# Performance work log

Measured on AMD Instinct MI355X. Metric: run time of the kernel, lower is better.

Reference implementation:

```python
import jax, jax.numpy as jnp
import numpy as np

N_ATOMS = 200000
N_BONDS = 300000
E = 600000
D = 128
H = 128
EPS = 1e-5  # BatchNorm1d default eps


def setup_inputs() -> dict:
    key = jax.random.key(0)
    ks = jax.random.split(key, 8)
    x_atoms = jax.random.normal(ks[0], (N_ATOMS, D), jnp.float32)
    x_bonds = jax.random.normal(ks[1], (N_BONDS, D), jnp.float32)
    # atoms -> bonds edges: row0 src atom idx, row1 dst bond idx
    ei_ab = jnp.stack([
        jax.random.randint(ks[2], (E,), 0, N_ATOMS),
        jax.random.randint(ks[3], (E,), 0, N_BONDS),
    ]).astype(jnp.int64)
    # bonds -> atoms edges
    ei_ba = jnp.stack([
        jax.random.randint(ks[4], (E,), 0, N_BONDS),
        jax.random.randint(ks[5], (E,), 0, N_ATOMS),
    ]).astype(jnp.int64)
    xav = float(np.sqrt(6.0 / (D + H)))
    W = jax.random.uniform(ks[6], (H, D), jnp.float32, -xav, xav)   # shared lin_rel
    b = jnp.zeros((H,), jnp.float32)
    Wr = jax.random.uniform(ks[7], (H, D), jnp.float32, -xav, xav)  # res_connection
    br = jnp.zeros((H,), jnp.float32)
    return {
        "x_atoms": x_atoms, "x_bonds": x_bonds,
        "ei_ab": ei_ab, "ei_ba": ei_ba,
        "W": W, "b": b, "Wr": Wr, "br": br,
        "gamma_atoms": jnp.ones((H,), jnp.float32),
        "beta_atoms": jnp.zeros((H,), jnp.float32),
        "gamma_bonds": jnp.ones((H,), jnp.float32),
        "beta_bonds": jnp.zeros((H,), jnp.float32),
    }


def _bn(v, g, bt):
    # BatchNorm1d training-mode math: batch mean, biased variance
    m = v.mean(axis=0)
    var = v.var(axis=0)
    return (v - m) * jax.lax.rsqrt(var + EPS) * g + bt


def reference(x_atoms, x_bonds, ei_ab, ei_ba, W, b, Wr, br,
              gamma_atoms, beta_atoms, gamma_bonds, beta_bonds):
    # shared lin_rel applied to both node types
    h_atoms = x_atoms @ W.T + b   # [N_ATOMS, H]
    h_bonds = x_bonds @ W.T + b   # [N_BONDS, H]

    # message = lin(x_src)[src], aggregate = scatter-add at dst (source_to_target)
    agg_bonds = jax.ops.segment_sum(h_atoms[ei_ab[0]], ei_ab[1], num_segments=N_BONDS)
    agg_atoms = jax.ops.segment_sum(h_bonds[ei_ba[0]], ei_ba[1], num_segments=N_ATOMS)

    # residual: activation(res_connection(x))
    out_atoms = agg_atoms + jax.nn.relu(x_atoms @ Wr.T + br)
    out_bonds = agg_bonds + jax.nn.relu(x_bonds @ Wr.T + br)

    # dropout is identity in eval/deterministic reference
    out_atoms = _bn(out_atoms, gamma_atoms, beta_atoms)
    out_bonds = _bn(out_bonds, gamma_bonds, beta_bonds)
    return out_atoms, out_bonds
```

## Files before the change

### kernel.cpp

```cpp
#include <hip/hip_runtime.h>
#include <stdint.h>

#define NATOMS 200000
#define NBONDS 300000
#define NEDGE  600000
#define NSEG   (NATOMS + NBONDS)
#define DF     128
#define EPS    1e-5f
#define SCHUNK 2048
#define NSBLK  ((NSEG + SCHUNK - 1) / SCHUNK)
#define NBUCK  32
#define NCHA   (NATOMS / 64)
#define NCHB   ((NBONDS + 63) / 64)
#define NCH    (NCHA + NCHB)

typedef __attribute__((ext_vector_type(8))) short bf16x8;
typedef __attribute__((ext_vector_type(4))) float f32x4;
typedef unsigned short u16;

__device__ __forceinline__ short f2b(float f) {
  union { float f; uint32_t u; } v; v.f = f;
  uint32_t r = v.u + 0x7fffu + ((v.u >> 16) & 1u);
  return (short)(r >> 16);
}
__device__ __forceinline__ float bf2f(u16 h) {
  union { uint32_t u; float f; } v; v.u = ((uint32_t)h) << 16; return v.f;
}
__device__ __forceinline__ bf16x8 pack8(float4 u, float4 v) {
  bf16x8 t;
  t[0] = f2b(u.x); t[1] = f2b(u.y); t[2] = f2b(u.z); t[3] = f2b(u.w);
  t[4] = f2b(v.x); t[5] = f2b(v.y); t[6] = f2b(v.z); t[7] = f2b(v.w);
  return t;
}

__global__ void k_prep(const float* __restrict__ W, const float* __restrict__ Wr,
                       u16* __restrict__ Wb, u16* __restrict__ Wrb) {
  int i = blockIdx.x * blockDim.x + threadIdx.x;
  if (i < DF * DF) {
    Wb[i]  = (u16)f2b(W[i]);
    Wrb[i] = (u16)f2b(Wr[i]);
  }
}

__global__ void k_setup(const float* __restrict__ xa, const float* __restrict__ xb,
                        u16* __restrict__ xaT, u16* __restrict__ xbT,
                        const int* __restrict__ ab, const int* __restrict__ ba,
                        int* __restrict__ cnt,
                        const float* __restrict__ W, const float* __restrict__ Wr,
                        u16* __restrict__ Wb, u16* __restrict__ Wrb) {
  const int NA8 = NATOMS * DF / 8;
  const int NT8 = NSEG * DF / 8;
  int bid = blockIdx.x;
  if (bid < 4096) {
    int stride = 4096 * 256;
    for (int i = bid * 256 + threadIdx.x; i < NT8; i += stride) {
      const float* src; u16* dst; int j;
      if (i < NA8) { src = xa; dst = xaT; j = i; }
      else { src = xb; dst = xbT; j = i - NA8; }
      const float4 a = *(const float4*)(src + (size_t)j * 8);
      const float4 b = *(const float4*)(src + (size_t)j * 8 + 4);
      *(bf16x8*)(dst + (size_t)j * 8) = pack8(a, b);
    }
  } else if (bid < 4608) {
    int stride = 512 * 256;
    for (int e = (bid - 4096) * 256 + threadIdx.x; e < 2 * NEDGE; e += stride) {
      int g;
      if (e < NEDGE) g = NATOMS + ab[NEDGE + e];
      else           g = ba[NEDGE + (e - NEDGE)];
      atomicAdd(cnt + g, 1);
    }
  } else {
    int i = (bid - 4608) * 256 + threadIdx.x;
    if (i < DF * DF) {
      Wb[i]  = (u16)f2b(W[i]);
      Wrb[i] = (u16)f2b(Wr[i]);
    }
  }
}

__global__ void k_hist(const int* __restrict__ ab, const int* __restrict__ ba,
                       int* __restrict__ cnt) {
  int stride = gridDim.x * blockDim.x;
  for (int e = blockIdx.x * blockDim.x + threadIdx.x; e < 2 * NEDGE; e += stride) {
    int g;
    if (e < NEDGE) g = NATOMS + ab[NEDGE + e];
    else           g = ba[NEDGE + (e - NEDGE)];
    atomicAdd(cnt + g, 1);
  }
}

__global__ void k_scanA(const int* __restrict__ cnt, int* __restrict__ bsum) {
  __shared__ int wsm[4];
  int t = threadIdx.x;
  int base = blockIdx.x * SCHUNK + t * 8;
  int s = 0;
#pragma unroll
  for (int j = 0; j < 8; ++j) { int i = base + j; if (i < NSEG) s += cnt[i]; }
  for (int d = 1; d < 64; d <<= 1) s += __shfl_xor(s, d);
  if ((t & 63) == 0) wsm[t >> 6] = s;
  __syncthreads();
  if (t == 0) bsum[blockIdx.x] = wsm[0] + wsm[1] + wsm[2] + wsm[3];
}

__global__ void k_scanB(const int* __restrict__ bsum, int* __restrict__ bbase) {
  __shared__ int wsm[4];
  int t = threadIdx.x;
  int lane = t & 63;
  int v = (t < NSBLK) ? bsum[t] : 0;
  int s = v;
  for (int d = 1; d < 64; d <<= 1) { int n = __shfl_up(s, d); if (lane >= d) s += n; }
  if (lane == 63) wsm[t >> 6] = s;
  __syncthreads();
  int wbase = 0;
  for (int w = 0; w < (t >> 6); ++w) wbase += wsm[w];
  if (t < NSBLK) bbase[t] = wbase + s - v;
}

__global__ void k_scanC(const int* __restrict__ cnt, const int* __restrict__ bbase,
                        int* __restrict__ off, int* __restrict__ cursor) {
  __shared__ int wsm[4];
  int t = threadIdx.x;
  int lane = t & 63, wv = t >> 6;
  int base = blockIdx.x * SCHUNK + t * 8;
  int v[8]; int ts = 0;
#pragma unroll
  for (int j = 0; j < 8; ++j) { int i = base + j; v[j] = (i < NSEG) ? cnt[i] : 0; ts += v[j]; }
  int s = ts;
  for (int d = 1; d < 64; d <<= 1) { int n = __shfl_up(s, d); if (lane >= d) s += n; }
  if (lane == 63) wsm[wv] = s;
  __syncthreads();
  int wbase = bbase[blockIdx.x];
  for (int w = 0; w < wv; ++w) wbase += wsm[w];
  int run = wbase + s - ts;
#pragma unroll
  for (int j = 0; j < 8; ++j) {
    int i = base + j;
    if (i < NSEG) { off[i] = run; cursor[i] = run; }
    run += v[j];
  }
}

__global__ void k_fill(const int* __restrict__ ab, const int* __restrict__ ba,
                       int* __restrict__ cursor, int* __restrict__ sorted) {
  int stride = gridDim.x * blockDim.x;
  for (int e = blockIdx.x * blockDim.x + threadIdx.x; e < 2 * NEDGE; e += stride) {
    int g, src;
    if (e < NEDGE) { g = NATOMS + ab[NEDGE + e]; src = ab[e]; }
    else { int e2 = e - NEDGE; g = ba[NEDGE + e2]; src = ba[e2]; }
    int pos = atomicAdd(cursor + g, 1);
    sorted[pos] = src;
  }
}

__global__ __launch_bounds__(256, 2) void k_fuse(
    const u16* __restrict__ xaT, const u16* __restrict__ xbT,
    const int* __restrict__ sorted, const int* __restrict__ off,
    const int* __restrict__ cnt, u16* __restrict__ gT,
    const u16* __restrict__ Wb, const u16* __restrict__ Wrb,
    const float* __restrict__ bb, const float* __restrict__ brb,
    float* __restrict__ stats) {
  __shared__ u16 aggL[64 * DF];

  int tid = threadIdx.x;
  int lane = tid & 63;
  int wv = tid >> 6;
  int r16 = lane & 15, kq = lane >> 4;
  int t016 = wv * 32;
  int qw = tid >> 4;
  int l16 = tid & 15;

  bf16x8 wf[2][4], wrf[2][4];
#pragma unroll
  for (int ti = 0; ti < 2; ++ti) {
#pragma unroll
    for (int kk = 0; kk < 4; ++kk) {
      size_t o = (size_t)(t016 + ti * 16 + r16) * DF + kk * 32 + kq * 8;
      wf[ti][kk]  = *(const bf16x8*)(Wb + o);
      wrf[ti][kk] = *(const bf16x8*)(Wrb + o);
    }
  }
  float bvv0 = bb[t016 + r16],      brr0 = brb[t016 + r16];
  float bvv1 = bb[t016 + 16 + r16], brr1 = brb[t016 + 16 + r16];

  float sA0 = 0.f, sA1 = 0.f, qA0 = 0.f, qA1 = 0.f;
  float sB0 = 0.f, sB1 = 0.f, qB0 = 0.f, qB1 = 0.f;

  for (int c = blockIdx.x; c < NCH; c += gridDim.x) {
    int typ, nrows, goff, base;
    if (c < NCHA) { typ = 0; nrows = NATOMS; goff = 0; base = c * 64; }
    else { typ = 1; nrows = NBONDS; goff = NATOMS; base = (c - NCHA) * 64; }
    const u16* gsrc = typ ? xaT : xbT;
    const u16* xsrc = typ ? xbT : xaT;

    __syncthreads();

#pragma unroll
    for (int i = 0; i < 4; ++i) {
      int r = qw + i * 16;
      int row = base + r;
      if (row < nrows) {
        int gidx = goff + row;
        int start = off[gidx], deg = cnt[gidx];
        float a0 = 0.f, a1 = 0.f, a2 = 0.f, a3 = 0.f;
        float a4 = 0.f, a5 = 0.f, a6 = 0.f, a7 = 0.f;
        int k = 0;
        for (; k + 1 < deg; k += 2) {
          int s0 = sorted[start + k], s1 = sorted[start + k + 1];
          bf16x8 v0 = *(const bf16x8*)(gsrc + (size_t)s0 * DF + l16 * 8);
          bf16x8 v1 = *(const bf16x8*)(gsrc + (size_t)s1 * DF + l16 * 8);
          a0 += bf2f((u16)v0[0]) + bf2f((u16)v1[0]);
          a1 += bf2f((u16)v0[1]) + bf2f((u16)v1[1]);
          a2 += bf2f((u16)v0[2]) + bf2f((u16)v1[2]);
          a3 += bf2f((u16)v0[3]) + bf2f((u16)v1[3]);
          a4 += bf2f((u16)v0[4]) + bf2f((u16)v1[4]);
          a5 += bf2f((u16)v0[5]) + bf2f((u16)v1[5]);
          a6 += bf2f((u16)v0[6]) + bf2f((u16)v1[6]);
          a7 += bf2f((u16)v0[7]) + bf2f((u16)v1[7]);
        }
        if (k < deg) {
          int s0 = sorted[start + k];
          bf16x8 v0 = *(const bf16x8*)(gsrc + (size_t)s0 * DF + l16 * 8);
          a0 += bf2f((u16)v0[0]); a1 += bf2f((u16)v0[1]);
          a2 += bf2f((u16)v0[2]); a3 += bf2f((u16)v0[3]);
          a4 += bf2f((u16)v0[4]); a5 += bf2f((u16)v0[5]);
          a6 += bf2f((u16)v0[6]); a7 += bf2f((u16)v0[7]);
        }
        bf16x8 rr;
        rr[0] = f2b(a0); rr[1] = f2b(a1); rr[2] = f2b(a2); rr[3] = f2b(a3);
        rr[4] = f2b(a4); rr[5] = f2b(a5); rr[6] = f2b(a6); rr[7] = f2b(a7);
        *(bf16x8*)(aggL + r * DF + ((l16 ^ (r & 7)) * 8)) = rr;
      }
    }
    __syncthreads();

#pragma unroll
    for (int rg = 0; rg < 4; ++rg) {
      int rowbase = base + rg * 16;
      if (rowbase < nrows) {
        int lrow = rg * 16 + r16;
        bf16x8 fA[4], fX[4];
#pragma unroll
        for (int kk = 0; kk < 4; ++kk) {
          int c8 = (4 * kk + kq) ^ (r16 & 7);
          fA[kk] = *(const bf16x8*)(aggL + lrow * DF + c8 * 8);
        }
        const u16* xp = xsrc + (size_t)(rowbase + r16) * DF + kq * 8;
#pragma unroll
        for (int kk = 0; kk < 4; ++kk) fX[kk] = *(const bf16x8*)(xp + kk * 32);

        f32x4 w0 = {0.f,0.f,0.f,0.f}, w1 = {0.f,0.f,0.f,0.f};
        f32x4 r0 = {0.f,0.f,0.f,0.f}, r1 = {0.f,0.f,0.f,0.f};
#pragma unroll
        for (int kk = 0; kk < 4; ++kk) {
          w0 = __builtin_amdgcn_mfma_f32_16x16x32_bf16(fA[kk], wf[0][kk], w0, 0, 0, 0);
          w1 = __builtin_amdgcn_mfma_f32_16x16x32_bf16(fA[kk], wf[1][kk], w1, 0, 0, 0);
          r0 = __builtin_amdgcn_mfma_f32_16x16x32_bf16(fX[kk], wrf[0][kk], r0, 0, 0, 0);
          r1 = __builtin_amdgcn_mfma_f32_16x16x32_bf16(fX[kk], wrf[1][kk], r1, 0, 0, 0);
        }

        float cf0 = (float)cnt[goff + rowbase + kq * 4 + 0];
        float cf1 = (float)cnt[goff + rowbase + kq * 4 + 1];
        float cf2 = (float)cnt[goff + rowbase + kq * 4 + 2];
        float cf3 = (float)cnt[goff + rowbase + kq * 4 + 3];

        u16* gp = gT + ((size_t)(goff + rowbase + kq * 4) << 7) + t016 + r16;
        float g0, g1, g2, g3, ss, qq;
        g0 = w0[0] + cf0 * bvv0 + fmaxf(r0[0] + brr0, 0.f);
        g1 = w0[1] + cf1 * bvv0 + fmaxf(r0[1] + brr0, 0.f);
        g2 = w0[2] + cf2 * bvv0 + fmaxf(r0[2] + brr0, 0.f);
        g3 = w0[3] + cf3 * bvv0 + fmaxf(r0[3] + brr0, 0.f);
        gp[0]   = (u16)f2b(g0); gp[128] = (u16)f2b(g1);
        gp[256] = (u16)f2b(g2); gp[384] = (u16)f2b(g3);
        ss = g0 + g1 + g2 + g3;
        qq = g0*g0 + g1*g1 + g2*g2 + g3*g3;
        if (typ) { sB0 += ss; qB0 += qq; } else { sA0 += ss; qA0 += qq; }
        g0 = w1[0] + cf0 * bvv1 + fmaxf(r1[0] + brr1, 0.f);
        g1 = w1[1] + cf1 * bvv1 + fmaxf(r1[1] + brr1, 0.f);
        g2 = w1[2] + cf2 * bvv1 + fmaxf(r1[2] + brr1, 0.f);
        g3 = w1[3] + cf3 * bvv1 + fmaxf(r1[3] + brr1, 0.f);
        gp[16]  = (u16)f2b(g0); gp[144] = (u16)f2b(g1);
        gp[272] = (u16)f2b(g2); gp[400] = (u16)f2b(g3);
        ss = g0 + g1 + g2 + g3;
        qq = g0*g0 + g1*g1 + g2*g2 + g3*g3;
        if (typ) { sB1 += ss; qB1 += qq; } else { sA1 += ss; qA1 += qq; }
      }
    }
  }

  int bkt = blockIdx.x & (NBUCK - 1);
  float* p = stats + (size_t)bkt * 4 * DF;
  {
    float s0 = sA0, q0 = qA0, s1 = sB0, q1 = qB0;
    s0 += __shfl_xor(s0, 16); q0 += __shfl_xor(q0, 16);
    s1 += __shfl_xor(s1, 16); q1 += __shfl_xor(q1, 16);
    s0 += __shfl_xor(s0, 32); q0 += __shfl_xor(q0, 32);
    s1 += __shfl_xor(s1, 32); q1 += __shfl_xor(q1, 32);
    if (kq == 0) {
      int feat = t016 + r16;
      atomicAdd(p + 0 * DF + feat, s0);
      atomicAdd(p + 1 * DF + feat, q0);
      atomicAdd(p + 2 * DF + feat, s1);
      atomicAdd(p + 3 * DF + feat, q1);
    }
  }
  {
    float s0 = sA1, q0 = qA1, s1 = sB1, q1 = qB1;
    s0 += __shfl_xor(s0, 16); q0 += __shfl_xor(q0, 16);
    s1 += __shfl_xor(s1, 16); q1 += __shfl_xor(q1, 16);
    s0 += __shfl_xor(s0, 32); q0 += __shfl_xor(q0, 32);
    s1 += __shfl_xor(s1, 32); q1 += __shfl_xor(q1, 32);
    if (kq == 0) {
      int feat = t016 + 16 + r16;
      atomicAdd(p + 0 * DF + feat, s0);
      atomicAdd(p + 1 * DF + feat, q0);
      atomicAdd(p + 2 * DF + feat, s1);
      atomicAdd(p + 3 * DF + feat, q1);
    }
  }
}

__global__ void k_gather_f(const float* __restrict__ xa, const float* __restrict__ xb,
                           const int* __restrict__ sorted, const int* __restrict__ off,
                           const int* __restrict__ cnt, float* __restrict__ outf) {
  int l32 = threadIdx.x & 31;
  int hwid = (blockIdx.x * blockDim.x + threadIdx.x) >> 5;
  int nhw = (gridDim.x * blockDim.x) >> 5;
  for (int g = hwid; g < NSEG; g += nhw) {
    int start = off[g], deg = cnt[g];
    const float* src = (g < NATOMS) ? xb : xa;
    float a0 = 0.f, a1 = 0.f, a2 = 0.f, a3 = 0.f;
    int k = 0;
    for (; k + 1 < deg; k += 2) {
      int s0 = sorted[start + k], s1 = sorted[start + k + 1];
      float4 v0 = *(const float4*)(src + (size_t)s0 * DF + l32 * 4);
      float4 v1 = *(const float4*)(src + (size_t)s1 * DF + l32 * 4);
      a0 += v0.x + v1.x; a1 += v0.y + v1.y; a2 += v0.z + v1.z; a3 += v0.w + v1.w;
    }
    if (k < deg) {
      int s0 = sorted[start + k];
      float4 v0 = *(const float4*)(src + (size_t)s0 * DF + l32 * 4);
      a0 += v0.x; a1 += v0.y; a2 += v0.z; a3 += v0.w;
    }
    float4 r; r.x = a0; r.y = a1; r.z = a2; r.w = a3;
    *(float4*)(outf + (size_t)g * DF + l32 * 4) = r;
  }
}

__global__ __launch_bounds__(256, 2) void k_gemm0(
    const float* __restrict__ xa, const float* __restrict__ xb,
    float* __restrict__ outf, const int* __restrict__ cnt,
    const u16* __restrict__ Wb, const u16* __restrict__ Wrb,
    const float* __restrict__ bb, const float* __restrict__ brb,
    float* __restrict__ stats) {
  int lane = threadIdx.x & 63;
  int wv = threadIdx.x >> 6;
  int r16 = lane & 15, kq = lane >> 4;
  int t016 = wv * 32;

  bf16x8 wf[2][4], wrf[2][4];
#pragma unroll
  for (int ti = 0; ti < 2; ++ti) {
#pragma unroll
    for (int kk = 0; kk < 4; ++kk) {
      size_t o = (size_t)(t016 + ti * 16 + r16) * DF + kk * 32 + kq * 8;
      wf[ti][kk]  = *(const bf16x8*)(Wb + o);
      wrf[ti][kk] = *(const bf16x8*)(Wrb + o);
    }
  }
  float bvv[2] = { bb[t016 + r16], bb[t016 + 16 + r16] };
  float brr[2] = { brb[t016 + r16], brb[t016 + 16 + r16] };

  float sA[2] = {0.f, 0.f}, qA[2] = {0.f, 0.f};
  float sB[2] = {0.f, 0.f}, qB[2] = {0.f, 0.f};

  for (int c = blockIdx.x; c < NCH; c += gridDim.x) {
    int typ, nrows, goff, base;
    if (c < NCHA) { typ = 0; nrows = NATOMS; goff = 0; base = c * 64; }
    else { typ = 1; nrows = NBONDS; goff = NATOMS; base = (c - NCHA) * 64; }
    const float* xsrc = typ ? xb : xa;

#pragma unroll
    for (int rg = 0; rg < 4; ++rg) {
      int rowbase = base + rg * 16;
      if (rowbase < nrows) {
        int row = rowbase + r16;
        const float* ap = outf + (size_t)(goff + row) * DF + kq * 8;
        const float* xp = xsrc + (size_t)row * DF + kq * 8;
        bf16x8 fA[4], fX[4];
#pragma unroll
        for (int kk = 0; kk < 4; ++kk) {
          fA[kk] = pack8(*(const float4*)(ap + kk * 32), *(const float4*)(ap + kk * 32 + 4));
          fX[kk] = pack8(*(const float4*)(xp + kk * 32), *(const float4*)(xp + kk * 32 + 4));
        }
        __syncthreads();

        f32x4 accW[2], accR[2];
#pragma unroll
        for (int ti = 0; ti < 2; ++ti) {
#pragma unroll
          for (int r = 0; r < 4; ++r) { accW[ti][r] = 0.f; accR[ti][r] = 0.f; }
        }
#pragma unroll
        for (int kk = 0; kk < 4; ++kk) {
#pragma unroll
          for (int ti = 0; ti < 2; ++ti) {
            accW[ti] = __builtin_amdgcn_mfma_f32_16x16x32_bf16(fA[kk], wf[ti][kk], accW[ti], 0, 0, 0);
            accR[ti] = __builtin_amdgcn_mfma_f32_16x16x32_bf16(fX[kk], wrf[ti][kk], accR[ti], 0, 0, 0);
          }
        }
        float cf[4];
#pragma unroll
        for (int r = 0; r < 4; ++r)
          cf[r] = (float)cnt[goff + rowbase + kq * 4 + r];
#pragma unroll
        for (int ti = 0; ti < 2; ++ti) {
          int feat = t016 + ti * 16 + r16;
          float s = 0.f, q = 0.f;
#pragma unroll
          for (int r = 0; r < 4; ++r) {
            int grow = rowbase + kq * 4 + r;
            float gg = accW[ti][r] + cf[r] * bvv[ti] + fmaxf(accR[ti][r] + brr[ti], 0.f);
            outf[(size_t)(goff + grow) * DF + feat] = gg;
            s += gg; q += gg * gg;
          }
          if (typ == 0) { sA[ti] += s; qA[ti] += q; }
          else          { sB[ti] += s; qB[ti] += q; }
        }
      }
    }
  }

  int bkt = blockIdx.x & (NBUCK - 1);
  float* p = stats + (size_t)bkt * 4 * DF;
#pragma unroll
  for (int ti = 0; ti < 2; ++ti) {
    float s0 = sA[ti], q0 = qA[ti], s1 = sB[ti], q1 = qB[ti];
    s0 += __shfl_xor(s0, 16); q0 += __shfl_xor(q0, 16);
    s1 += __shfl_xor(s1, 16); q1 += __shfl_xor(q1, 16);
    s0 += __shfl_xor(s0, 32); q0 += __shfl_xor(q0, 32);
    s1 += __shfl_xor(s1, 32); q1 += __shfl_xor(q1, 32);
    if (kq == 0) {
      int feat = t016 + ti * 16 + r16;
      atomicAdd(p + 0 * DF + feat, s0);
      atomicAdd(p + 1 * DF + feat, q0);
      atomicAdd(p + 2 * DF + feat, s1);
      atomicAdd(p + 3 * DF + feat, q1);
    }
  }
}

__global__ void k_stats(const float* __restrict__ stats,
                        const float* __restrict__ ga, const float* __restrict__ bea,
                        const float* __restrict__ gb, const float* __restrict__ beb,
                        float* __restrict__ scale, float* __restrict__ shift) {
  int tid = threadIdx.x;
  if (tid < 2 * DF) {
    int t = tid >> 7, f = tid & (DF - 1);
    float S = 0.f, SS = 0.f;
    for (int bk = 0; bk < NBUCK; ++bk) {
      const float* p = stats + (size_t)bk * 4 * DF;
      S  += p[(2 * t) * DF + f];
      SS += p[(2 * t + 1) * DF + f];
    }
    float n = t ? (float)NBONDS : (float)NATOMS;
    float mean = S / n;
    float var = SS / n - mean * mean;
    float rstd = rsqrtf(var + EPS);
    float g = t ? gb[f] : ga[f];
    float be = t ? beb[f] : bea[f];
    scale[tid] = rstd * g;
    shift[tid] = be - mean * rstd * g;
  }
}

template<int TIER>
__global__ void k_norm(float* __restrict__ out, const u16* __restrict__ gT,
                       const float* __restrict__ scale, const float* __restrict__ shift) {
  if constexpr (TIER) {
    const size_t nv = (size_t)NSEG * DF / 8;
    size_t stride = (size_t)gridDim.x * blockDim.x;
    for (size_t i = (size_t)blockIdx.x * blockDim.x + threadIdx.x; i < nv; i += stride) {
      size_t e = i * 8;
      int t = e >= (size_t)NATOMS * DF;
      int f = (int)(e & (DF - 1));
      bf16x8 v = *(const bf16x8*)(gT + e);
      const float* sc = scale + t * DF + f;
      const float* sh = shift + t * DF + f;
      float4 o0, o1;
      o0.x = fmaf(bf2f((u16)v[0]), sc[0], sh[0]);
      o0.y = fmaf(bf2f((u16)v[1]), sc[1], sh[1]);
      o0.z = fmaf(bf2f((u16)v[2]), sc[2], sh[2]);
      o0.w = fmaf(bf2f((u16)v[3]), sc[3], sh[3]);
      o1.x = fmaf(bf2f((u16)v[4]), sc[4], sh[4]);
      o1.y = fmaf(bf2f((u16)v[5]), sc[5], sh[5]);
      o1.z = fmaf(bf2f((u16)v[6]), sc[6], sh[6]);
      o1.w = fmaf(bf2f((u16)v[7]), sc[7], sh[7]);
      *(float4*)(out + e) = o0;
      *(float4*)(out + e + 4) = o1;
    }
  } else {
    const size_t nv = (size_t)NSEG * DF / 4;
    size_t stride = (size_t)gridDim.x * blockDim.x;
    for (size_t i = (size_t)blockIdx.x * blockDim.x + threadIdx.x; i < nv; i += stride) {
      size_t e = i * 4;
      int t = e >= (size_t)NATOMS * DF;
      int f = (int)(e & (DF - 1));
      const float* sc = scale + t * DF + f;
      const float* sh = shift + t * DF + f;
      float4 v = ((float4*)out)[i];
      v.x = fmaf(v.x, sc[0], sh[0]);
      v.y = fmaf(v.y, sc[1], sh[1]);
      v.z = fmaf(v.z, sc[2], sh[2]);
      v.w = fmaf(v.w, sc[3], sh[3]);
      ((float4*)out)[i] = v;
    }
  }
}

extern "C" void kernel_launch(void* const* d_in, const int* in_sizes, int n_in,
                              void* d_out, int out_size, void* d_ws, size_t ws_size,
                              hipStream_t stream) {
  const float* xa  = (const float*)d_in[0];
  const float* xb  = (const float*)d_in[1];
  const int*   ab  = (const int*)d_in[2];
  const int*   ba  = (const int*)d_in[3];
  const float* W   = (const float*)d_in[4];
  const float* b   = (const float*)d_in[5];
  const float* Wr  = (const float*)d_in[6];
  const float* br  = (const float*)d_in[7];
  const float* ga  = (const float*)d_in[8];
  const float* bea = (const float*)d_in[9];
  const float* gb  = (const float*)d_in[10];
  const float* beb = (const float*)d_in[11];
  float* out = (float*)d_out;

  char* ws = (char*)d_ws;
  int*   cnt    = (int*)ws;
  int*   off    = (int*)(ws +  2000000);
  int*   cursor = (int*)(ws +  4000000);
  int*   sorted = (int*)(ws +  6000000);
  float* stats  = (float*)(ws + 10800000);
  int*   bsum   = (int*)(ws + 10865536);
  int*   bbase  = (int*)(ws + 10866560);
  u16*   Wbf    = (u16*)(ws + 10867584);
  u16*   Wrbf   = (u16*)(ws + 10900352);
  float* scale  = (float*)(ws + 10933120);
  float* shift  = (float*)(ws + 10934144);
  u16*   gT   = (u16*)(ws + 10935168);
  u16*   xaT  = (u16*)(ws + 138935168);
  u16*   xbT  = (u16*)(ws + 190135168);
  const bool xt = ws_size >= 266935168ull;

  hipMemsetAsync(cnt, 0, 2000000, stream);
  hipMemsetAsync(stats, 0, 65536, stream);

  if (xt) {
    k_setup<<<4672, 256, 0, stream>>>(xa, xb, xaT, xbT, ab, ba, cnt, W, Wr, Wbf, Wrbf);
  } else {
    k_prep<<<64, 256, 0, stream>>>(W, Wr, Wbf, Wrbf);
    k_hist<<<2048, 256, 0, stream>>>(ab, ba, cnt);
  }
  k_scanA<<<NSBLK, 256, 0, stream>>>(cnt, bsum);
  k_scanB<<<1, 256, 0, stream>>>(bsum, bbase);
  k_scanC<<<NSBLK, 256, 0, stream>>>(cnt, bbase, off, cursor);
  k_fill<<<2048, 256, 0, stream>>>(ab, ba, cursor, sorted);

  if (xt) {
    k_fuse<<<2048, 256, 0, stream>>>(xaT, xbT, sorted, off, cnt, gT,
                                     Wbf, Wrbf, b, br, stats);
    k_stats<<<1, 256, 0, stream>>>(stats, ga, bea, gb, beb, scale, shift);
    k_norm<1><<<4096, 256, 0, stream>>>(out, gT, scale, shift);
  } else {
    k_gather_f<<<8192, 256, 0, stream>>>(xa, xb, sorted, off, cnt, out);
    k_gemm0<<<2048, 256, 0, stream>>>(xa, xb, out, cnt, Wbf, Wrbf, b, br, stats);
    k_stats<<<1, 256, 0, stream>>>(stats, ga, bea, gb, beb, scale, shift);
    k_norm<0><<<8192, 256, 0, stream>>>(out, gT, scale, shift);
  }
}
```

Before: 550.7 us.

## Stage edge indices in LDS and gather rows with one wave per row

```diff
diff --git a/kernel.cpp b/kernel.cpp
--- a/kernel.cpp
+++ b/kernel.cpp
@@ -13,6 +13,7 @@
 #define NCHA   (NATOMS / 64)
 #define NCHB   ((NBONDS + 63) / 64)
 #define NCH    (NCHA + NCHB)
+#define IDXCAP 1024
 
 typedef __attribute__((ext_vector_type(8))) short bf16x8;
 typedef __attribute__((ext_vector_type(4))) float f32x4;
@@ -25,6 +26,9 @@
 }
 __device__ __forceinline__ float bf2f(u16 h) {
   union { uint32_t u; float f; } v; v.u = ((uint32_t)h) << 16; return v.f;
+}
+__device__ __forceinline__ float u2f(uint32_t u) {
+  union { uint32_t u; float f; } v; v.u = u; return v.f;
 }
 __device__ __forceinline__ bf16x8 pack8(float4 u, float4 v) {
   bf16x8 t;
@@ -160,14 +164,15 @@
     const float* __restrict__ bb, const float* __restrict__ brb,
     float* __restrict__ stats) {
   __shared__ u16 aggL[64 * DF];
+  __shared__ int idxL[IDXCAP];
+  __shared__ int offL[64];
+  __shared__ int cntL[64];
 
   int tid = threadIdx.x;
   int lane = tid & 63;
   int wv = tid >> 6;
   int r16 = lane & 15, kq = lane >> 4;
   int t016 = wv * 32;
-  int qw = tid >> 4;
-  int l16 = tid & 15;
 
   bf16x8 wf[2][4], wrf[2][4];
 #pragma unroll
@@ -191,44 +196,52 @@
     else { typ = 1; nrows = NBONDS; goff = NATOMS; base = (c - NCHA) * 64; }
     const u16* gsrc = typ ? xaT : xbT;
     const u16* xsrc = typ ? xbT : xaT;
+    int gbase = goff + base;
 
     __syncthreads();
 
-#pragma unroll
-    for (int i = 0; i < 4; ++i) {
-      int r = qw + i * 16;
-      int row = base + r;
-      if (row < nrows) {
-        int gidx = goff + row;
-        int start = off[gidx], deg = cnt[gidx];
-        float a0 = 0.f, a1 = 0.f, a2 = 0.f, a3 = 0.f;
-        float a4 = 0.f, a5 = 0.f, a6 = 0.f, a7 = 0.f;
+    if (tid < 64) {
+      int ok = (base + tid) < nrows;
+      offL[tid] = ok ? off[gbase + tid] : 0;
+      cntL[tid] = ok ? cnt[gbase + tid] : 0;
+    }
+    __syncthreads();
+
+    int lastr = min(nrows - base, 64) - 1;
+    int wstart = offL[0];
+    int wlen = offL[lastr] + cntL[lastr] - wstart;
+    int wcap = wlen < IDXCAP ? wlen : IDXCAP;
+    for (int w = tid; w < wcap; w += 256) idxL[w] = sorted[wstart + w];
+    __syncthreads();
+
+#pragma unroll 2
+    for (int i = 0; i < 16; ++i) {
+      int r = wv * 16 + i;
+      if (base + r < nrows) {
+        int srel = offL[r] - wstart;
+        int deg = cntL[r];
+        const u16* rowp = gsrc + lane * 2;
+        float aLo0 = 0.f, aHi0 = 0.f, aLo1 = 0.f, aHi1 = 0.f;
         int k = 0;
         for (; k + 1 < deg; k += 2) {
-          int s0 = sorted[start + k], s1 = sorted[start + k + 1];
-          bf16x8 v0 = *(const bf16x8*)(gsrc + (size_t)s0 * DF + l16 * 8);
-          bf16x8 v1 = *(const bf16x8*)(gsrc + (size_t)s1 * DF + l16 * 8);
-          a0 += bf2f((u16)v0[0]) + bf2f((u16)v1[0]);
-          a1 += bf2f((u16)v0[1]) + bf2f((u16)v1[1]);
-          a2 += bf2f((u16)v0[2]) + bf2f((u16)v1[2]);
-          a3 += bf2f((u16)v0[3]) + bf2f((u16)v1[3]);
-          a4 += bf2f((u16)v0[4]) + bf2f((u16)v1[4]);
-          a5 += bf2f((u16)v0[5]) + bf2f((u16)v1[5]);
-          a6 += bf2f((u16)v0[6]) + bf2f((u16)v1[6]);
-          a7 += bf2f((u16)v0[7]) + bf2f((u16)v1[7]);
+          int w0 = srel + k;
+          int i0 = (w0 < IDXCAP) ? idxL[w0] : sorted[wstart + w0];
+          int i1 = (w0 + 1 < IDXCAP) ? idxL[w0 + 1] : sorted[wstart + w0 + 1];
+          uint32_t v0 = *(const uint32_t*)(rowp + (size_t)i0 * DF);
+          uint32_t v1 = *(const uint32_t*)(rowp + (size_t)i1 * DF);
+          aLo0 += u2f(v0 << 16); aHi0 += u2f(v0 & 0xffff0000u);
+          aLo1 += u2f(v1 << 16); aHi1 += u2f(v1 & 0xffff0000u);
         }
         if (k < deg) {
-          int s0 = sorted[start + k];
-          bf16x8 v0 = *(const bf16x8*)(gsrc + (size_t)s0 * DF + l16 * 8);
-          a0 += bf2f((u16)v0[0]); a1 += bf2f((u16)v0[1]);
-          a2 += bf2f((u16)v0[2]); a3 += bf2f((u16)v0[3]);
-          a4 += bf2f((u16)v0[4]); a5 += bf2f((u16)v0[5]);
-          a6 += bf2f((u16)v0[6]); a7 += bf2f((u16)v0[7]);
-        }
-        bf16x8 rr;
-        rr[0] = f2b(a0); rr[1] = f2b(a1); rr[2] = f2b(a2); rr[3] = f2b(a3);
-        rr[4] = f2b(a4); rr[5] = f2b(a5); rr[6] = f2b(a6); rr[7] = f2b(a7);
-        *(bf16x8*)(aggL + r * DF + ((l16 ^ (r & 7)) * 8)) = rr;
+          int w0 = srel + k;
+          int i0 = (w0 < IDXCAP) ? idxL[w0] : sorted[wstart + w0];
+          uint32_t v0 = *(const uint32_t*)(rowp + (size_t)i0 * DF);
+          aLo0 += u2f(v0 << 16); aHi0 += u2f(v0 & 0xffff0000u);
+        }
+        float aLo = aLo0 + aLo1, aHi = aHi0 + aHi1;
+        uint32_t pk = (uint32_t)(u16)f2b(aLo) | ((uint32_t)(u16)f2b(aHi) << 16);
+        int cc = (lane >> 2) ^ (i & 7);
+        *(uint32_t*)((char*)aggL + r * 256 + cc * 16 + (lane & 3) * 4) = pk;
       }
     }
     __syncthreads();
@@ -258,10 +271,10 @@
           r1 = __builtin_amdgcn_mfma_f32_16x16x32_bf16(fX[kk], wrf[1][kk], r1, 0, 0, 0);
         }
 
-        float cf0 = (float)cnt[goff + rowbase + kq * 4 + 0];
-        float cf1 = (float)cnt[goff + rowbase + kq * 4 + 1];
-        float cf2 = (float)cnt[goff + rowbase + kq * 4 + 2];
-        float cf3 = (float)cnt[goff + rowbase + kq * 4 + 3];
+        float cf0 = (float)cntL[rg * 16 + kq * 4 + 0];
+        float cf1 = (float)cntL[rg * 16 + kq * 4 + 1];
+        float cf2 = (float)cntL[rg * 16 + kq * 4 + 2];
+        float cf3 = (float)cntL[rg * 16 + kq * 4 + 3];
 
         u16* gp = gT + ((size_t)(goff + rowbase + kq * 4) << 7) + t016 + r16;
         float g0, g1, g2, g3, ss, qq;
```

Measured after the change: 584.7 us. +6.2%, slower.
